# Performance work log

Measured on AMD Instinct MI355X. Metric: run time of the kernel, lower is better.

Reference implementation:

```python
import jax, jax.numpy as jnp
import numpy as np

T, B = 256, 128
VOCAB, EMB, HID, LABELS = 50257, 1024, 1024, 50


def setup_inputs() -> dict:
    key = jax.random.key(0)
    ks = jax.random.split(key, 6)
    sentence = jax.random.randint(ks[0], (T, B), 0, VOCAB)
    emb = jax.random.normal(ks[1], (VOCAB, EMB), dtype=jnp.float32) * 0.02
    W = jax.random.normal(ks[2], (EMB, 3 * HID), dtype=jnp.float32) * (1.0 / np.sqrt(EMB))
    b = jnp.zeros((3 * HID,), dtype=jnp.float32)
    Wout = jax.random.normal(ks[3], (HID, LABELS), dtype=jnp.float32) * (1.0 / np.sqrt(HID))
    bout = jnp.zeros((LABELS,), dtype=jnp.float32)
    return {"sentence": sentence, "emb": emb, "W": W, "b": b, "Wout": Wout, "bout": bout}


def reference(sentence, emb, W, b, Wout, bout):
    # Embedding lookup: [T, B, EMB]
    x = emb[sentence]
    # QRNN gate projection (window=1): [T, B, 3H]
    y = jnp.einsum('tbe,eh->tbh', x, W) + b
    z, f, o = jnp.split(y, 3, axis=-1)
    z = jnp.tanh(z)
    f = jax.nn.sigmoid(f)
    o = jax.nn.sigmoid(o)

    # fo-pool recurrence: c_t = f_t * z_t + (1 - f_t) * c_{t-1}, c_0 = 0
    def step(c, zf):
        z_t, f_t = zf
        c = f_t * z_t + (1.0 - f_t) * c
        return c, c

    c0 = jnp.zeros((B, HID), dtype=z.dtype)
    _, C = jax.lax.scan(step, c0, (z, f))
    # hidden output at last timestep: h_T = o_T * c_T
    h_last = o[-1] * C[-1]  # [B, HID]
    logits = h_last @ Wout + bout  # [B, LABELS]
    return jax.nn.log_softmax(logits, axis=-1)
```

## Files before the change

### kernel.cpp

```cpp
#include <hip/hip_runtime.h>
#include <hip/hip_bf16.h>

#define T_LEN 256
#define B_DIM 128
#define EMB 1024
#define HID 1024
#define NLAB 50
#define M_ROWS (T_LEN * B_DIM)
#define N3H 3072
#define KT 32

typedef __attribute__((ext_vector_type(8))) short short8;
typedef __attribute__((ext_vector_type(4))) float f32x4;

static __device__ __forceinline__ ushort f2b(float x) {
    unsigned u = __builtin_bit_cast(unsigned, x);
    unsigned lsb = (u >> 16) & 1u;
    u += 0x7fffu + lsb;
    return (ushort)(u >> 16);
}
static __device__ __forceinline__ float b2f(ushort u) {
    unsigned v = ((unsigned)u) << 16;
    return __builtin_bit_cast(float, v);
}
static __device__ __forceinline__ void gload16(const ushort* g, ushort* l) {
    __builtin_amdgcn_global_load_lds(
        (const __attribute__((address_space(1))) unsigned int*)g,
        (__attribute__((address_space(3))) unsigned int*)l,
        16, 0, 0);
}
static __device__ __forceinline__ float fast_sigmoid(float y) {
    return 1.f / (1.f + __expf(-y));
}
static __device__ __forceinline__ float fast_tanh(float y) {
    float e = __expf(2.f * y);
    return (e - 1.f) / (e + 1.f);
}

__global__ __launch_bounds__(256) void gather_convert(
    const int* __restrict__ sent, const float* __restrict__ emb,
    ushort* __restrict__ xb)
{
    const int row = blockIdx.x * 16 + (threadIdx.x >> 4);
    const int seg = threadIdx.x & 15;
    const size_t src = (size_t)sent[row] * EMB;
    const float4* ep = (const float4*)(emb + src);
    ushort4* op = (ushort4*)(xb + (size_t)row * EMB);
#pragma unroll
    for (int j = 0; j < 16; j++) {
        float4 v = ep[seg + j * 16];
        ushort4 o;
        o.x = f2b(v.x); o.y = f2b(v.y); o.z = f2b(v.z); o.w = f2b(v.w);
        op[seg + j * 16] = o;
    }
}

__global__ __launch_bounds__(256) void transposeW(
    const float* __restrict__ W, ushort* __restrict__ Wt)
{
    __shared__ float tile[32][33];
    const int n0 = blockIdx.x * 32, k0 = blockIdx.y * 32;
    const int tx = threadIdx.x, ty = threadIdx.y;
#pragma unroll
    for (int j = 0; j < 32; j += 8)
        tile[ty + j][tx] = W[(size_t)(k0 + ty + j) * N3H + n0 + tx];
    __syncthreads();
#pragma unroll
    for (int j = 0; j < 32; j += 8)
        Wt[(size_t)(n0 + ty + j) * EMB + k0 + tx] = f2b(tile[tx][ty + j]);
}

__global__ __launch_bounds__(256) void gemm128(
    const ushort* __restrict__ A, const ushort* __restrict__ Bt,
    const float* __restrict__ bias,
    ushort* __restrict__ zb, ushort* __restrict__ fb, ushort* __restrict__ ob)
{
    __shared__ ushort LA[128 * 32];
    __shared__ ushort LB[128 * 32];

    const int tid = threadIdx.x;
    const int lane = tid & 63;
    const int w = tid >> 6;
    const int wr = w >> 1, wc = w & 1;
    const int l15 = lane & 15, lh = lane >> 4;

    const int wg = blockIdx.x;
    const ushort *Ab, *Bb;
    const float* bptr;
    ushort* dst;
    int rowbase, colbase;
    bool use_tanh;
    if (wg < 4096) {
        const int w2 = (wg & 7) * 512 + (wg >> 3);
        const int mt = w2 >> 4, nt = w2 & 15;
        Ab = A + (size_t)mt * 128 * EMB;
        Bb = Bt + (size_t)nt * 128 * EMB;
        bptr = bias + nt * 128;
        rowbase = mt * 128;
        if (nt < 8) { dst = zb; colbase = nt * 128; use_tanh = true; }
        else        { dst = fb; colbase = (nt - 8) * 128; use_tanh = false; }
    } else {
        const int q = wg - 4096;
        Ab = A + (size_t)(M_ROWS - 128) * EMB;
        Bb = Bt + (size_t)(2048 + q * 128) * EMB;
        bptr = bias + 2048 + q * 128;
        rowbase = 0; colbase = q * 128;
        dst = ob; use_tanh = false;
    }

    const int r0 = tid >> 2, g0 = tid & 3;
    const int r1 = (tid + 256) >> 2, g1 = tid & 3;
    const ushort* gA0 = Ab + (size_t)r0 * EMB + g0 * 8;
    const ushort* gA1 = Ab + (size_t)r1 * EMB + g1 * 8;
    const ushort* gB0 = Bb + (size_t)r0 * EMB + g0 * 8;
    const ushort* gB1 = Bb + (size_t)r1 * EMB + g1 * 8;
    ushort* lA0 = LA + tid * 8;
    ushort* lA1 = LA + (tid + 256) * 8;
    ushort* lB0 = LB + tid * 8;
    ushort* lB1 = LB + (tid + 256) * 8;

    int adA[4], adB[4];
#pragma unroll
    for (int mi = 0; mi < 4; mi++)
        adA[mi] = (wr * 64 + mi * 16 + l15) * 32 + lh * 8;
#pragma unroll
    for (int ni = 0; ni < 4; ni++)
        adB[ni] = (wc * 64 + ni * 16 + l15) * 32 + lh * 8;

    f32x4 acc[4][4] = {};

    for (int kk = 0; kk < KT; ++kk) {
        const int ko = kk * 32;
        gload16(gA0 + ko, lA0);
        gload16(gA1 + ko, lA1);
        gload16(gB0 + ko, lB0);
        gload16(gB1 + ko, lB1);
        __syncthreads();

        short8 af[4], bf[4];
#pragma unroll
        for (int i = 0; i < 4; i++) {
            af[i] = *(const short8*)&LA[adA[i]];
            bf[i] = *(const short8*)&LB[adB[i]];
        }
#pragma unroll
        for (int mi = 0; mi < 4; mi++)
#pragma unroll
            for (int ni = 0; ni < 4; ni++)
                acc[mi][ni] = __builtin_amdgcn_mfma_f32_16x16x32_bf16(
                    af[mi], bf[ni], acc[mi][ni], 0, 0, 0);
        __syncthreads();
    }

#pragma unroll
    for (int mi = 0; mi < 4; mi++) {
#pragma unroll
        for (int ni = 0; ni < 4; ni++) {
            const int nb = wc * 64 + ni * 16 + l15;
            const float bv = bptr[nb];
            const int rl = wr * 64 + mi * 16 + lh * 4;
#pragma unroll
            for (int r = 0; r < 4; r++) {
                float y = acc[mi][ni][r] + bv;
                float a = use_tanh ? fast_tanh(y) : fast_sigmoid(y);
                dst[(size_t)(rowbase + rl + r) * HID + colbase + nb] = f2b(a);
            }
        }
    }
}

__global__ __launch_bounds__(256) void fo_pool(
    const unsigned* __restrict__ z32, const unsigned* __restrict__ fz32,
    const unsigned* __restrict__ o32, float* __restrict__ hbuf)
{
    const int p = blockIdx.x * 256 + threadIdx.x;
    float c0 = 0.f, c1 = 0.f;
#pragma unroll 8
    for (int t = 0; t < T_LEN; ++t) {
        unsigned zz = z32[(size_t)t * (B_DIM * HID / 2) + p];
        unsigned ff = fz32[(size_t)t * (B_DIM * HID / 2) + p];
        float z0 = b2f((ushort)(zz & 0xffffu)), z1 = b2f((ushort)(zz >> 16));
        float f0 = b2f((ushort)(ff & 0xffffu)), f1 = b2f((ushort)(ff >> 16));
        c0 += f0 * (z0 - c0);
        c1 += f1 * (z1 - c1);
    }
    unsigned oo = o32[p];
    float o0 = b2f((ushort)(oo & 0xffffu)), o1 = b2f((ushort)(oo >> 16));
    hbuf[2 * p]     = o0 * c0;
    hbuf[2 * p + 1] = o1 * c1;
}

__global__ __launch_bounds__(64) void classify(
    const float* __restrict__ hbuf, const float* __restrict__ Wout,
    const float* __restrict__ bout, float* __restrict__ out)
{
    __shared__ float hs[HID];
    const int b = blockIdx.x, l = threadIdx.x;
#pragma unroll
    for (int j = 0; j < HID; j += 64) hs[j + l] = hbuf[(size_t)b * HID + j + l];
    __syncthreads();
    float acc = -1e30f;
    if (l < NLAB) {
        float s = bout[l];
#pragma unroll 4
        for (int e = 0; e < HID; e++) s += hs[e] * Wout[(size_t)e * NLAB + l];
        acc = s;
    }
    float m = acc;
#pragma unroll
    for (int off = 32; off; off >>= 1) m = fmaxf(m, __shfl_xor(m, off));
    float ex = (l < NLAB) ? expf(acc - m) : 0.f;
    float sum = ex;
#pragma unroll
    for (int off = 32; off; off >>= 1) sum += __shfl_xor(sum, off);
    if (l < NLAB) out[(size_t)b * NLAB + l] = acc - m - logf(sum);
}

extern "C" void kernel_launch(void* const* d_in, const int* in_sizes, int n_in,
                              void* d_out, int out_size, void* d_ws, size_t ws_size,
                              hipStream_t stream) {
    const int* sent = (const int*)d_in[0];
    const float* emb = (const float*)d_in[1];
    const float* W = (const float*)d_in[2];
    const float* bias = (const float*)d_in[3];
    const float* Wout = (const float*)d_in[4];
    const float* bout = (const float*)d_in[5];
    float* out = (float*)d_out;

    ushort* xb = (ushort*)d_ws;
    ushort* Wt = xb + (size_t)M_ROWS * EMB;
    ushort* zb = Wt + (size_t)N3H * EMB;
    ushort* fb = zb + (size_t)M_ROWS * HID;
    ushort* ob = fb + (size_t)M_ROWS * HID;
    float* hb = (float*)(ob + (size_t)B_DIM * HID);

    hipLaunchKernelGGL(gather_convert, dim3(M_ROWS / 16), dim3(256), 0, stream,
                       sent, emb, xb);
    hipLaunchKernelGGL(transposeW, dim3(N3H / 32, EMB / 32), dim3(32, 8), 0, stream,
                       W, Wt);
    hipLaunchKernelGGL(gemm128, dim3(4096 + 8), dim3(256), 0, stream,
                       xb, Wt, bias, zb, fb, ob);
    hipLaunchKernelGGL(fo_pool, dim3(B_DIM * HID / 2 / 256), dim3(256), 0, stream,
                       (const unsigned*)zb, (const unsigned*)fb,
                       (const unsigned*)ob, hb);
    hipLaunchKernelGGL(classify, dim3(B_DIM), dim3(64), 0, stream,
                       hb, Wout, bout, out);
}
```

Before: 352.5 us.

## Double GEMM K-tile to 64 with XOR-swizzled LDS layout

```diff
diff --git a/kernel.cpp b/kernel.cpp
--- a/kernel.cpp
+++ b/kernel.cpp
@@ -8,7 +8,7 @@
 #define NLAB 50
 #define M_ROWS (T_LEN * B_DIM)
 #define N3H 3072
-#define KT 32
+#define KT 16
 
 typedef __attribute__((ext_vector_type(8))) short short8;
 typedef __attribute__((ext_vector_type(4))) float f32x4;
@@ -75,8 +75,8 @@
     const float* __restrict__ bias,
     ushort* __restrict__ zb, ushort* __restrict__ fb, ushort* __restrict__ ob)
 {
-    __shared__ ushort LA[128 * 32];
-    __shared__ ushort LB[128 * 32];
+    __shared__ ushort LA[128 * 64];
+    __shared__ ushort LB[128 * 64];
 
     const int tid = threadIdx.x;
     const int lane = tid & 63;
@@ -108,47 +108,74 @@
         dst = ob; use_tanh = false;
     }
 
-    const int r0 = tid >> 2, g0 = tid & 3;
-    const int r1 = (tid + 256) >> 2, g1 = tid & 3;
-    const ushort* gA0 = Ab + (size_t)r0 * EMB + g0 * 8;
-    const ushort* gA1 = Ab + (size_t)r1 * EMB + g1 * 8;
-    const ushort* gB0 = Bb + (size_t)r0 * EMB + g0 * 8;
-    const ushort* gB1 = Bb + (size_t)r1 * EMB + g1 * 8;
-    ushort* lA0 = LA + tid * 8;
-    ushort* lA1 = LA + (tid + 256) * 8;
-    ushort* lB0 = LB + tid * 8;
-    ushort* lB1 = LB + (tid + 256) * 8;
-
-    int adA[4], adB[4];
-#pragma unroll
-    for (int mi = 0; mi < 4; mi++)
-        adA[mi] = (wr * 64 + mi * 16 + l15) * 32 + lh * 8;
-#pragma unroll
-    for (int ni = 0; ni < 4; ni++)
-        adB[ni] = (wc * 64 + ni * 16 + l15) * 32 + lh * 8;
+    const ushort* gA[4];
+    const ushort* gB[4];
+    int dOf[4];
+#pragma unroll
+    for (int q = 0; q < 4; q++) {
+        const int c = q * 256 + tid;
+        const int row = c >> 3;
+        const int gsrc = (c & 7) ^ (row & 7);
+        gA[q] = Ab + (size_t)row * EMB + gsrc * 8;
+        gB[q] = Bb + (size_t)row * EMB + gsrc * 8;
+        dOf[q] = c * 8;
+    }
+
+    const int swz0 = (lh ^ (l15 & 7)) * 8;
+    const int swz1 = ((4 + lh) ^ (l15 & 7)) * 8;
+    const int aRow = (wr * 64 + l15) * 64;
+    const int bRow = (wc * 64 + l15) * 64;
 
     f32x4 acc[4][4] = {};
 
     for (int kk = 0; kk < KT; ++kk) {
-        const int ko = kk * 32;
-        gload16(gA0 + ko, lA0);
-        gload16(gA1 + ko, lA1);
-        gload16(gB0 + ko, lB0);
-        gload16(gB1 + ko, lB1);
+        const int ko = kk * 64;
+        gload16(gA[0] + ko, LA + dOf[0]);
+        gload16(gA[1] + ko, LA + dOf[1]);
+        gload16(gA[2] + ko, LA + dOf[2]);
+        gload16(gA[3] + ko, LA + dOf[3]);
+        gload16(gB[0] + ko, LB + dOf[0]);
+        gload16(gB[1] + ko, LB + dOf[1]);
+        gload16(gB[2] + ko, LB + dOf[2]);
+        gload16(gB[3] + ko, LB + dOf[3]);
         __syncthreads();
 
-        short8 af[4], bf[4];
-#pragma unroll
-        for (int i = 0; i < 4; i++) {
-            af[i] = *(const short8*)&LA[adA[i]];
-            bf[i] = *(const short8*)&LB[adB[i]];
+        {
+            short8 a0 = *(const short8*)&LA[aRow + swz0];
+            short8 a1 = *(const short8*)&LA[aRow + 1024 + swz0];
+            short8 a2 = *(const short8*)&LA[aRow + 2048 + swz0];
+            short8 a3 = *(const short8*)&LA[aRow + 3072 + swz0];
+            short8 b0 = *(const short8*)&LB[bRow + swz0];
+            short8 b1 = *(const short8*)&LB[bRow + 1024 + swz0];
+            short8 b2 = *(const short8*)&LB[bRow + 2048 + swz0];
+            short8 b3 = *(const short8*)&LB[bRow + 3072 + swz0];
+#pragma unroll
+            for (int mi = 0; mi < 4; mi++) {
+                const short8 am = (mi == 0) ? a0 : (mi == 1) ? a1 : (mi == 2) ? a2 : a3;
+                acc[mi][0] = __builtin_amdgcn_mfma_f32_16x16x32_bf16(am, b0, acc[mi][0], 0, 0, 0);
+                acc[mi][1] = __builtin_amdgcn_mfma_f32_16x16x32_bf16(am, b1, acc[mi][1], 0, 0, 0);
+                acc[mi][2] = __builtin_amdgcn_mfma_f32_16x16x32_bf16(am, b2, acc[mi][2], 0, 0, 0);
+                acc[mi][3] = __builtin_amdgcn_mfma_f32_16x16x32_bf16(am, b3, acc[mi][3], 0, 0, 0);
+            }
         }
-#pragma unroll
-        for (int mi = 0; mi < 4; mi++)
-#pragma unroll
-            for (int ni = 0; ni < 4; ni++)
-                acc[mi][ni] = __builtin_amdgcn_mfma_f32_16x16x32_bf16(
-                    af[mi], bf[ni], acc[mi][ni], 0, 0, 0);
+        {
+            short8 a0 = *(const short8*)&LA[aRow + swz1];
+            short8 a1 = *(const short8*)&LA[aRow + 1024 + swz1];
+            short8 a2 = *(const short8*)&LA[aRow + 2048 + swz1];
+            short8 a3 = *(const short8*)&LA[aRow + 3072 + swz1];
+            short8 b0 = *(const short8*)&LB[bRow + swz1];
+            short8 b1 = *(const short8*)&LB[bRow + 1024 + swz1];
+            short8 b2 = *(const short8*)&LB[bRow + 2048 + swz1];
+            short8 b3 = *(const short8*)&LB[bRow + 3072 + swz1];
+#pragma unroll
+            for (int mi = 0; mi < 4; mi++) {
+                const short8 am = (mi == 0) ? a0 : (mi == 1) ? a1 : (mi == 2) ? a2 : a3;
+                acc[mi][0] = __builtin_amdgcn_mfma_f32_16x16x32_bf16(am, b0, acc[mi][0], 0, 0, 0);
+                acc[mi][1] = __builtin_amdgcn_mfma_f32_16x16x32_bf16(am, b1, acc[mi][1], 0, 0, 0);
+                acc[mi][2] = __builtin_amdgcn_mfma_f32_16x16x32_bf16(am, b2, acc[mi][2], 0, 0, 0);
+                acc[mi][3] = __builtin_amdgcn_mfma_f32_16x16x32_bf16(am, b3, acc[mi][3], 0, 0, 0);
+            }
+        }
         __syncthreads();
     }
 
```

Measured after the change: 324.7 us. -7.9%, faster.
